# Performance work log

Measured on AMD Instinct MI355X. Metric: run time of the kernel, lower is better.

The kernel has to match this reference:

```python
import jax, jax.numpy as jnp
import numpy as np
from functools import partial

L, B, D_IN, D_MODEL, D_OUT, D_STATE = 2048, 8, 128, 256, 32, 16
D_INNER, DT_RANK, K_CONV = 2 * D_MODEL, D_MODEL // 16, 4
LOG2PI = float(np.log(2.0 * np.pi))


def setup_inputs() -> dict:
    key = jax.random.key(0)
    ks = jax.random.split(key, 16)
    sc = 0.02
    inp = {
        "s": jax.random.normal(ks[0], (L, B, D_IN), jnp.float32),
        "a": jax.random.normal(ks[1], (L, B, D_OUT), jnp.float32),
        # embedding linear
        "W_emb": jax.random.normal(ks[2], (D_IN, D_MODEL), jnp.float32) * sc,
        "b_emb": jnp.zeros((D_MODEL,), jnp.float32),
        # mamba block params
        "norm_w": jnp.ones((D_MODEL,), jnp.float32),
        "W_in": jax.random.normal(ks[3], (D_MODEL, 2 * D_INNER), jnp.float32) * sc,
        "conv_w": jax.random.normal(ks[4], (D_INNER, 1, K_CONV), jnp.float32) * sc,
        "conv_b": jnp.zeros((D_INNER,), jnp.float32),
        "W_x": jax.random.normal(ks[5], (D_INNER, DT_RANK + 2 * D_STATE), jnp.float32) * sc,
        "W_dt": jax.random.normal(ks[6], (DT_RANK, D_INNER), jnp.float32) * sc,
        "b_dt": jnp.full((D_INNER,), -2.0, jnp.float32),  # softplus(-2) ~ small init dt
        "A_log": jnp.broadcast_to(jnp.log(jnp.arange(1, D_STATE + 1, dtype=jnp.float32)), (D_INNER, D_STATE)).copy(),
        "D": jnp.ones((D_INNER,), jnp.float32),
        "W_out": jax.random.normal(ks[7], (D_INNER, D_MODEL), jnp.float32) * sc,
        # action head + log_std
        "W_head": jax.random.normal(ks[8], (D_MODEL, D_OUT), jnp.float32) * sc,
        "b_head": jnp.zeros((D_OUT,), jnp.float32),
        "log_std": jnp.zeros((D_OUT,), jnp.float32),
    }
    return inp


def _rmsnorm(x, w, eps=1e-5):
    return x * jax.lax.rsqrt(jnp.mean(x * x, axis=-1, keepdims=True) + eps) * w


def _silu(x):
    return x * jax.nn.sigmoid(x)


def _mamba_block(x, norm_w, W_in, conv_w, conv_b, W_x, W_dt, b_dt, A_log, D, W_out):
    # x: (B, L, d_model)
    resid = x
    xn = _rmsnorm(x, norm_w)
    xz = xn @ W_in                                  # (B, L, 2*d_inner)
    xp, z = jnp.split(xz, 2, axis=-1)
    # causal depthwise conv over time
    xc = jax.lax.conv_general_dilated(
        xp.transpose(0, 2, 1), conv_w, window_strides=(1,),
        padding=[(K_CONV - 1, 0)], feature_group_count=D_INNER,
        dimension_numbers=("NCH", "OIH", "NCH"))
    xp = _silu((xc + conv_b[None, :, None]).transpose(0, 2, 1))  # (B, L, d_inner)
    # input-dependent SSM params
    x_dbl = xp @ W_x                                # (B, L, dt_rank + 2*d_state)
    dt, Bm, Cm = jnp.split(x_dbl, [DT_RANK, DT_RANK + D_STATE], axis=-1)
    dt = jax.nn.softplus(dt @ W_dt + b_dt)          # (B, L, d_inner)
    A = -jnp.exp(A_log)                             # (d_inner, d_state)

    def step(h, t):
        dt_t, B_t, C_t, x_t = t                     # (B,d_i) (B,d_s) (B,d_s) (B,d_i)
        dA = jnp.exp(dt_t[..., None] * A)           # (B, d_inner, d_state)
        dBx = (dt_t * x_t)[..., None] * B_t[:, None, :]
        h = dA * h + dBx
        y = jnp.einsum("bds,bs->bd", h, C_t)
        return h, y

    h0 = jnp.zeros((x.shape[0], D_INNER, D_STATE), x.dtype)
    tm = lambda u: jnp.moveaxis(u, 1, 0)            # time-major
    _, ys = jax.lax.scan(step, h0, (tm(dt), tm(Bm), tm(Cm), tm(xp)))
    y = jnp.moveaxis(ys, 0, 1) + xp * D             # (B, L, d_inner)
    y = y * _silu(z)
    return y @ W_out + resid


def reference(s, a, W_emb, b_emb, norm_w, W_in, conv_w, conv_b, W_x, W_dt, b_dt,
              A_log, D, W_out, W_head, b_head, log_std):
    x = s @ W_emb + b_emb                           # (L, B, d_model)
    x = x.transpose(1, 0, 2)                        # (B, L, d_model)
    x = _mamba_block(x, norm_w, W_in, conv_w, conv_b, W_x, W_dt, b_dt, A_log, D, W_out)
    x = x.transpose(1, 0, 2)                        # (L, B, d_model)
    mu = x @ W_head + b_head                        # (L, B, d_out)
    # Normal(mu, exp(log_std)).log_prob(a).sum(-1)
    z = (a - mu) * jnp.exp(-log_std)
    logp = -0.5 * z * z - log_std - 0.5 * LOG2PI
    return logp.sum(axis=-1)                        # (L, B)
```

## Files before the change

### kernel.cpp

```cpp
#include <hip/hip_runtime.h>

typedef unsigned short u16;
typedef short bf16x8 __attribute__((ext_vector_type(8)));
typedef float floatx4 __attribute__((ext_vector_type(4)));

#define LSEQ 2048
#define BB 8
#define NTOK (LSEQ*BB)
#define DMODEL 256
#define DINNER 512
#define NSEG 128
#define SEGLEN 16

__device__ __forceinline__ float siluf(float x){ return x / (1.f + __expf(-x)); }
__device__ __forceinline__ float b2f(u16 x){ return __uint_as_float(((unsigned)x) << 16); }
__device__ __forceinline__ u16 f2b(float f){
  unsigned u = __float_as_uint(f);
  unsigned r = (u + 0x7fffu + ((u >> 16) & 1u)) >> 16;
  return (u16)r;
}

__global__ __launch_bounds__(256) void prep_k(
    const float* __restrict__ Wemb, const float* __restrict__ Win,
    const float* __restrict__ Wout, const float* __restrict__ Wx,
    const float* __restrict__ Wdt, const float* __restrict__ Wh,
    u16* __restrict__ WTe, u16* __restrict__ WTi, u16* __restrict__ WTo,
    u16* __restrict__ WxT, u16* __restrict__ WdtTp, u16* __restrict__ WhT)
{
  int g = blockIdx.x, tid = threadIdx.x;
  if (g < 128) {
    int idx = g*256 + tid; int n = idx >> 7, k = idx & 127;
    WTe[idx] = f2b(Wemb[(size_t)k*256 + n]);
  } else if (g < 1152) {
    int idx = (g-128)*256 + tid; int n = idx >> 8, k = idx & 255;
    WTi[idx] = f2b(Win[(size_t)k*1024 + n]);
  } else if (g < 1664) {
    int idx = (g-1152)*256 + tid; int n = idx >> 9, k = idx & 511;
    WTo[idx] = f2b(Wout[(size_t)k*256 + n]);
  } else if (g < 1760) {
    int idx = (g-1664)*256 + tid; int n = idx >> 9, k = idx & 511;
    WxT[idx] = f2b(Wx[(size_t)k*48 + n]);
  } else if (g < 1824) {
    int idx = (g-1760)*256 + tid; int c = idx >> 5, r = idx & 31;
    WdtTp[idx] = (r < 16) ? f2b(Wdt[(size_t)r*512 + c]) : (u16)0;
  } else {
    int idx = (g-1824)*256 + tid; int j = idx >> 8, k = idx & 255;
    WhT[idx] = f2b(Wh[(size_t)k*32 + j]);
  }
}

__global__ __launch_bounds__(256) void embnorm_k(
    const float* __restrict__ s, const u16* __restrict__ WTe,
    const float* __restrict__ bemb, const float* __restrict__ nw,
    u16* __restrict__ Xb, u16* __restrict__ XNb)
{
  __shared__ u16 SH[64*264];
  __shared__ float ssq[64*4];
  __shared__ float rr[64];
  u16* As = SH;
  u16* Bs = SH + 64*40;
  const int tid = threadIdx.x;
  const int wave = tid >> 6, lane = tid & 63;
  const int quad = lane >> 4, l16 = lane & 15;
  const int m0 = blockIdx.x*64;
  const int wn = wave*64;
  const int srow = tid >> 2, sch = (tid & 3)*8;
  floatx4 acc[4][4];
  #pragma unroll
  for (int r = 0; r < 4; ++r)
    #pragma unroll
    for (int c = 0; c < 4; ++c) acc[r][c] = (floatx4){0.f,0.f,0.f,0.f};

  for (int k0 = 0; k0 < 128; k0 += 32) {
    {
      float4 v0 = *(const float4*)&s[(size_t)(m0+srow)*128 + k0 + sch];
      float4 v1 = *(const float4*)&s[(size_t)(m0+srow)*128 + k0 + sch + 4];
      __align__(16) u16 o[8];
      o[0]=f2b(v0.x); o[1]=f2b(v0.y); o[2]=f2b(v0.z); o[3]=f2b(v0.w);
      o[4]=f2b(v1.x); o[5]=f2b(v1.y); o[6]=f2b(v1.z); o[7]=f2b(v1.w);
      *(uint4*)&As[srow*40 + sch] = *(const uint4*)o;
    }
    #pragma unroll
    for (int p = 0; p < 4; ++p) {
      int row = srow + p*64;
      *(uint4*)&Bs[row*40 + sch] = *(const uint4*)&WTe[(size_t)row*128 + k0 + sch];
    }
    __syncthreads();
    bf16x8 af[4], bf[4];
    #pragma unroll
    for (int r = 0; r < 4; ++r) af[r] = *(const bf16x8*)&As[(r*16 + l16)*40 + quad*8];
    #pragma unroll
    for (int c = 0; c < 4; ++c) bf[c] = *(const bf16x8*)&Bs[(wn + c*16 + l16)*40 + quad*8];
    #pragma unroll
    for (int r = 0; r < 4; ++r)
      #pragma unroll
      for (int c = 0; c < 4; ++c)
        acc[r][c] = __builtin_amdgcn_mfma_f32_16x16x32_bf16(af[r], bf[c], acc[r][c], 0, 0, 0);
    __syncthreads();
  }
  u16* Xs = SH;
  #pragma unroll
  for (int c = 0; c < 4; ++c) {
    int n = wn + c*16 + l16;
    float bv = bemb[n];
    #pragma unroll
    for (int r = 0; r < 4; ++r)
      #pragma unroll
      for (int reg = 0; reg < 4; ++reg) {
        int ml = r*16 + quad*4 + reg;
        Xs[ml*264 + n] = f2b(acc[r][c][reg] + bv);
      }
  }
  __syncthreads();
  #pragma unroll
  for (int p = 0; p < 8; ++p) {
    int row = p*8 + (tid >> 5);
    int col = (tid & 31)*8;
    *(uint4*)&Xb[(size_t)(m0+row)*256 + col] = *(const uint4*)&Xs[row*264 + col];
  }
  const int tk = tid >> 2, q = tid & 3;
  float ss = 0.f;
  #pragma unroll
  for (int j = 0; j < 8; ++j) {
    uint4 v = *(const uint4*)&Xs[tk*264 + q*64 + j*8];
    const u16* u = (const u16*)&v;
    #pragma unroll
    for (int i = 0; i < 8; ++i) { float x = b2f(u[i]); ss += x*x; }
  }
  ssq[tk*4 + q] = ss;
  __syncthreads();
  if (q == 0)
    rr[tk] = rsqrtf((ssq[tk*4]+ssq[tk*4+1]+ssq[tk*4+2]+ssq[tk*4+3])*(1.f/DMODEL) + 1e-5f);
  __syncthreads();
  float r = rr[tk];
  #pragma unroll
  for (int j = 0; j < 8; ++j) {
    int idx = q*64 + j*8;
    uint4 v = *(const uint4*)&Xs[tk*264 + idx];
    const u16* u = (const u16*)&v;
    float4 w0 = *(const float4*)&nw[idx];
    float4 w1 = *(const float4*)&nw[idx+4];
    __align__(16) u16 o[8];
    o[0]=f2b(b2f(u[0])*r*w0.x); o[1]=f2b(b2f(u[1])*r*w0.y);
    o[2]=f2b(b2f(u[2])*r*w0.z); o[3]=f2b(b2f(u[3])*r*w0.w);
    o[4]=f2b(b2f(u[4])*r*w1.x); o[5]=f2b(b2f(u[5])*r*w1.y);
    o[6]=f2b(b2f(u[6])*r*w1.z); o[7]=f2b(b2f(u[7])*r*w1.w);
    *(uint4*)&XNb[(size_t)(m0+tk)*256 + idx] = *(const uint4*)o;
  }
}

template<int K>
__global__ __launch_bounds__(256) void gemm_mfma(
    const u16* __restrict__ Ab, const u16* __restrict__ WT,
    u16* __restrict__ Cv, int N)
{
  __shared__ u16 SH[128*136];
  u16* As = SH;
  u16* Bs = SH + 128*40;
  const int tid = threadIdx.x;
  const int wave = tid >> 6, lane = tid & 63;
  const int quad = lane >> 4, l16 = lane & 15;
  const int bm0 = blockIdx.x*128, bn0 = blockIdx.y*128;
  const int wm = (wave & 1)*64, wn = (wave >> 1)*64;
  const int srow = tid >> 2, sch = (tid & 3)*8;
  floatx4 acc[4][4];
  #pragma unroll
  for (int r = 0; r < 4; ++r)
    #pragma unroll
    for (int c = 0; c < 4; ++c) acc[r][c] = (floatx4){0.f,0.f,0.f,0.f};

  for (int k0 = 0; k0 < K; k0 += 32) {
    #pragma unroll
    for (int p = 0; p < 2; ++p) {
      int row = srow + p*64;
      *(uint4*)&As[row*40 + sch] = *(const uint4*)&Ab[(size_t)(bm0+row)*K + k0 + sch];
      *(uint4*)&Bs[row*40 + sch] = *(const uint4*)&WT[(size_t)(bn0+row)*K + k0 + sch];
    }
    __syncthreads();
    bf16x8 af[4], bf[4];
    #pragma unroll
    for (int r = 0; r < 4; ++r) af[r] = *(const bf16x8*)&As[(wm + r*16 + l16)*40 + quad*8];
    #pragma unroll
    for (int c = 0; c < 4; ++c) bf[c] = *(const bf16x8*)&Bs[(wn + c*16 + l16)*40 + quad*8];
    #pragma unroll
    for (int r = 0; r < 4; ++r)
      #pragma unroll
      for (int c = 0; c < 4; ++c)
        acc[r][c] = __builtin_amdgcn_mfma_f32_16x16x32_bf16(af[r], bf[c], acc[r][c], 0, 0, 0);
    __syncthreads();
  }
  u16* Cs = SH;
  #pragma unroll
  for (int c = 0; c < 4; ++c) {
    int nl = wn + c*16 + l16;
    #pragma unroll
    for (int r = 0; r < 4; ++r)
      #pragma unroll
      for (int reg = 0; reg < 4; ++reg) {
        int ml = wm + r*16 + quad*4 + reg;
        Cs[ml*136 + nl] = f2b(acc[r][c][reg]);
      }
  }
  __syncthreads();
  #pragma unroll
  for (int p = 0; p < 8; ++p) {
    int row = p*16 + (tid >> 4);
    int col = (tid & 15)*8;
    uint4 v = *(const uint4*)&Cs[row*136 + col];
    *(uint4*)&Cv[(size_t)(bm0+row)*N + bn0 + col] = v;
  }
}

__global__ __launch_bounds__(256) void xdblBC_k(const u16* __restrict__ XZb,
    const float* __restrict__ cw, const float* __restrict__ cb,
    const u16* __restrict__ WxT,
    float* __restrict__ BM, float* __restrict__ CM, u16* __restrict__ DTRb)
{
  __shared__ u16 As[64*40];
  __shared__ u16 Ws[48*40];
  __shared__ float CWs[512*4];
  __shared__ float CBs[512];
  const int tid = threadIdx.x;
  const int wave = tid >> 6, lane = tid & 63;
  const int quad = lane >> 4, l16 = lane & 15;
  const int m0 = blockIdx.x*64;
  const int srow = tid >> 2, sch = (tid & 3)*8;
  const int n = m0 + srow;
  for (int e = tid; e < 2048; e += 256) CWs[e] = cw[e];
  for (int e = tid; e < 512;  e += 256) CBs[e] = cb[e];
  floatx4 acc[3];
  #pragma unroll
  for (int j = 0; j < 3; ++j) acc[j] = (floatx4){0.f,0.f,0.f,0.f};
  __syncthreads();
  const bf16x8 z8 = {0,0,0,0,0,0,0,0};
  for (int k0 = 0; k0 < DINNER; k0 += 32) {
    bf16x8 t3 = *(const bf16x8*)&XZb[(size_t)n*1024 + k0 + sch];
    bf16x8 t2 = z8, t1 = z8, t0v = z8;
    if (n >= 8)  t2  = *(const bf16x8*)&XZb[(size_t)(n-8)*1024  + k0 + sch];
    if (n >= 16) t1  = *(const bf16x8*)&XZb[(size_t)(n-16)*1024 + k0 + sch];
    if (n >= 24) t0v = *(const bf16x8*)&XZb[(size_t)(n-24)*1024 + k0 + sch];
    __align__(16) u16 outa[8];
    #pragma unroll
    for (int j = 0; j < 8; ++j) {
      int c = k0 + sch + j;
      float4 wv = *(const float4*)&CWs[c*4];
      float xc = CBs[c] + wv.x*b2f((u16)t0v[j]) + wv.y*b2f((u16)t1[j])
               + wv.z*b2f((u16)t2[j]) + wv.w*b2f((u16)t3[j]);
      outa[j] = f2b(siluf(xc));
    }
    *(uint4*)&As[srow*40 + sch] = *(const uint4*)outa;
    if (tid < 192) {
      int wr = tid >> 2;
      *(uint4*)&Ws[wr*40 + sch] = *(const uint4*)&WxT[(size_t)wr*512 + k0 + sch];
    }
    __syncthreads();
    bf16x8 af = *(const bf16x8*)&As[(wave*16 + l16)*40 + quad*8];
    #pragma unroll
    for (int j = 0; j < 3; ++j) {
      bf16x8 bf = *(const bf16x8*)&Ws[(j*16 + l16)*40 + quad*8];
      acc[j] = __builtin_amdgcn_mfma_f32_16x16x32_bf16(af, bf, acc[j], 0, 0, 0);
    }
    __syncthreads();
  }
  const int tok0 = m0 + wave*16;
  #pragma unroll
  for (int reg = 0; reg < 4; ++reg) {
    size_t t = (size_t)(tok0 + quad*4 + reg);
    BM[t*16 + l16] = acc[1][reg];
    CM[t*16 + l16] = acc[2][reg];
    DTRb[t*32 + l16]      = f2b(acc[0][reg]);
    DTRb[t*32 + 16 + l16] = 0;
  }
}

__global__ __launch_bounds__(256) void dtg_k(const u16* __restrict__ DTRb,
    const u16* __restrict__ WdtTp, const float* __restrict__ bdt,
    u16* __restrict__ DTb)
{
  __shared__ u16 Cs[128*136];
  const int tid = threadIdx.x;
  const int wave = tid >> 6, lane = tid & 63;
  const int quad = lane >> 4, l16 = lane & 15;
  const int bm0 = blockIdx.x*128, bn0 = blockIdx.y*128;
  const int bm = bm0 + (wave & 1)*64;
  const int bn = bn0 + (wave >> 1)*64;
  bf16x8 af[4], bf[4];
  #pragma unroll
  for (int r = 0; r < 4; ++r)
    af[r] = *(const bf16x8*)(DTRb + (size_t)(bm + r*16 + l16)*32 + quad*8);
  #pragma unroll
  for (int c = 0; c < 4; ++c)
    bf[c] = *(const bf16x8*)(WdtTp + (size_t)(bn + c*16 + l16)*32 + quad*8);
  #pragma unroll
  for (int c = 0; c < 4; ++c) {
    int nl = (wave >> 1)*64 + c*16 + l16;
    float bd = bdt[bn0 + nl];
    #pragma unroll
    for (int r = 0; r < 4; ++r) {
      floatx4 d = __builtin_amdgcn_mfma_f32_16x16x32_bf16(af[r], bf[c],
                    (floatx4){0.f,0.f,0.f,0.f}, 0, 0, 0);
      #pragma unroll
      for (int reg = 0; reg < 4; ++reg) {
        int ml = (wave & 1)*64 + r*16 + quad*4 + reg;
        float sum = d[reg] + bd;
        Cs[ml*136 + nl] = f2b((sum > 20.f) ? sum : __logf(1.f + __expf(sum)));
      }
    }
  }
  __syncthreads();
  #pragma unroll
  for (int p = 0; p < 8; ++p) {
    int row = p*16 + (tid >> 4);
    int col = (tid & 15)*8;
    uint4 v = *(const uint4*)&Cs[row*136 + col];
    *(uint4*)&DTb[(size_t)(bm0+row)*DINNER + bn0 + col] = v;
  }
}

__global__ __launch_bounds__(256) void scanA_k(const u16* __restrict__ DTb,
    const u16* __restrict__ XZb, const float* __restrict__ BM,
    const float* __restrict__ cw, const float* __restrict__ cb,
    const float* __restrict__ Alog, u16* __restrict__ HENDb, float* __restrict__ DTS)
{
  __shared__ __align__(16) float Bs[SEGLEN*16];
  const int tid = threadIdx.x;
  const int seg = blockIdx.x, b = blockIdx.y, half = blockIdx.z;
  const int c = half*256 + tid;
  const int t0 = seg*SEGLEN;
  {
    int t = tid >> 4, s = tid & 15;
    Bs[tid] = BM[((size_t)(t0+t)*BB + b)*16 + s];
  }
  float As[16];
  #pragma unroll
  for (int s = 0; s < 16; ++s) As[s] = -__expf(Alog[c*16+s]);
  bool uni = true;
  #pragma unroll
  for (int s = 1; s < 16; ++s)
    uni = uni && (fabsf(As[s] - As[0]*(float)(s+1)) <= 1e-4f*(float)(s+1));
  const float4 cwv = *(const float4*)&cw[c*4];
  const float cbv = cb[c];
  float h[16];
  #pragma unroll
  for (int s = 0; s < 16; ++s) h[s] = 0.f;
  float dts = 0.f;
  __syncthreads();
  const size_t base = (size_t)t0*BB + b;
  const u16* dtp = DTb + base*DINNER + c;
  const u16* xzp = XZb + base*1024 + c;
  float w0 = (t0 >= 3) ? b2f(xzp[-(size_t)3*BB*1024]) : 0.f;
  float w1 = (t0 >= 2) ? b2f(xzp[-(size_t)2*BB*1024]) : 0.f;
  float w2 = (t0 >= 1) ? b2f(xzp[-(size_t)1*BB*1024]) : 0.f;
  float dt = b2f(dtp[0]);
  float xz = b2f(xzp[0]);
  for (int t = 0; t < SEGLEN; ++t) {
    float dtn = 0.f, xzn = 0.f;
    if (t+1 < SEGLEN) {
      dtn = b2f(dtp[(size_t)(t+1)*BB*DINNER]);
      xzn = b2f(xzp[(size_t)(t+1)*BB*1024]);
    }
    float xp = siluf(cbv + cwv.x*w0 + cwv.y*w1 + cwv.z*w2 + cwv.w*xz);
    w0 = w1; w1 = w2; w2 = xz;
    dts += dt;
    float dtx = dt * xp;
    const float4 b0 = *(const float4*)&Bs[t*16+0];
    const float4 b1 = *(const float4*)&Bs[t*16+4];
    const float4 b2 = *(const float4*)&Bs[t*16+8];
    const float4 b3 = *(const float4*)&Bs[t*16+12];
    const float bv[16] = {b0.x,b0.y,b0.z,b0.w, b1.x,b1.y,b1.z,b1.w,
                          b2.x,b2.y,b2.z,b2.w, b3.x,b3.y,b3.z,b3.w};
    float dA[16];
    if (uni) {
      float p = __expf(dt*As[0]);
      dA[0] = p;
      #pragma unroll
      for (int s = 1; s < 16; ++s) dA[s] = dA[s-1]*p;
    } else {
      #pragma unroll
      for (int s = 0; s < 16; ++s) dA[s] = __expf(dt*As[s]);
    }
    #pragma unroll
    for (int s = 0; s < 16; ++s)
      h[s] = fmaf(dA[s], h[s], dtx*bv[s]);
    dt = dtn; xz = xzn;
  }
  u16* hp = &HENDb[(((size_t)seg*BB + b)*DINNER + c)*16];
  #pragma unroll
  for (int q = 0; q < 2; ++q) {
    ushort4 v0, v1;
    v0.x = f2b(h[q*8+0]); v0.y = f2b(h[q*8+1]); v0.z = f2b(h[q*8+2]); v0.w = f2b(h[q*8+3]);
    v1.x = f2b(h[q*8+4]); v1.y = f2b(h[q*8+5]); v1.z = f2b(h[q*8+6]); v1.w = f2b(h[q*8+7]);
    *(ushort4*)&hp[q*8]     = v0;
    *(ushort4*)&hp[q*8 + 4] = v1;
  }
  DTS[((size_t)seg*BB + b)*DINNER + c] = dts;
}

__global__ __launch_bounds__(256) void stitch_k(u16* __restrict__ HENDb,
    const float* __restrict__ DTS, const float* __restrict__ Alog)
{
  int g = blockIdx.x*256 + threadIdx.x;
  int b = g >> 13;
  int rem = g & 8191;
  int cidx = rem >> 4;
  float A = -__expf(Alog[rem]);
  float h0 = 0.f;
  for (int k = 0; k < NSEG; ++k) {
    size_t idx = (((size_t)k*BB + b) << 13) + rem;
    float hend = b2f(HENDb[idx]);
    HENDb[idx] = f2b(h0);
    float dts = DTS[((size_t)k*BB + b)*DINNER + cidx];
    h0 = fmaf(__expf(dts*A), h0, hend);
  }
}

__global__ __launch_bounds__(256) void scanC_k(const u16* __restrict__ DTb,
    const u16* __restrict__ XZb, const float* __restrict__ BM, const float* __restrict__ CM,
    const float* __restrict__ cw, const float* __restrict__ cb,
    const float* __restrict__ Alog, const float* __restrict__ Dp,
    const u16* __restrict__ H0b, u16* __restrict__ YGb)
{
  __shared__ __align__(16) float Bs[SEGLEN*16];
  __shared__ __align__(16) float Cs[SEGLEN*16];
  const int tid = threadIdx.x;
  const int seg = blockIdx.x, b = blockIdx.y, half = blockIdx.z;
  const int c = half*256 + tid;
  const int t0 = seg*SEGLEN;
  {
    int t = tid >> 4, s = tid & 15;
    size_t nb = ((size_t)(t0+t)*BB + b)*16 + s;
    Bs[tid] = BM[nb];
    Cs[tid] = CM[nb];
  }
  float As[16];
  #pragma unroll
  for (int s = 0; s < 16; ++s) As[s] = -__expf(Alog[c*16+s]);
  bool uni = true;
  #pragma unroll
  for (int s = 1; s < 16; ++s)
    uni = uni && (fabsf(As[s] - As[0]*(float)(s+1)) <= 1e-4f*(float)(s+1));
  const float4 cwv = *(const float4*)&cw[c*4];
  const float cbv = cb[c];
  float h[16];
  const u16* hp = &H0b[(((size_t)seg*BB + b)*DINNER + c)*16];
  #pragma unroll
  for (int q = 0; q < 4; ++q) {
    ushort4 hv = *(const ushort4*)&hp[q*4];
    h[q*4+0]=b2f(hv.x); h[q*4+1]=b2f(hv.y); h[q*4+2]=b2f(hv.z); h[q*4+3]=b2f(hv.w);
  }
  const float Dv = Dp[c];
  __syncthreads();
  const size_t base = (size_t)t0*BB + b;
  const u16* dtp = DTb + base*DINNER + c;
  const u16* xzp = XZb + base*1024 + c;
  const u16* zp  = XZb + base*1024 + DINNER + c;
  u16*       ygp = YGb + base*DINNER + c;
  float w0 = (t0 >= 3) ? b2f(xzp[-(size_t)3*BB*1024]) : 0.f;
  float w1 = (t0 >= 2) ? b2f(xzp[-(size_t)2*BB*1024]) : 0.f;
  float w2 = (t0 >= 1) ? b2f(xzp[-(size_t)1*BB*1024]) : 0.f;
  float dt = b2f(dtp[0]);
  float xz = b2f(xzp[0]);
  float zg = b2f(zp[0]);
  for (int t = 0; t < SEGLEN; ++t) {
    float dtn = 0.f, xzn = 0.f, zgn = 0.f;
    if (t+1 < SEGLEN) {
      dtn = b2f(dtp[(size_t)(t+1)*BB*DINNER]);
      xzn = b2f(xzp[(size_t)(t+1)*BB*1024]);
      zgn = b2f(zp[(size_t)(t+1)*BB*1024]);
    }
    float xp = siluf(cbv + cwv.x*w0 + cwv.y*w1 + cwv.z*w2 + cwv.w*xz);
    w0 = w1; w1 = w2; w2 = xz;
    float dtx = dt * xp;
    const float4 b0 = *(const float4*)&Bs[t*16+0];
    const float4 b1 = *(const float4*)&Bs[t*16+4];
    const float4 b2 = *(const float4*)&Bs[t*16+8];
    const float4 b3 = *(const float4*)&Bs[t*16+12];
    const float4 c0 = *(const float4*)&Cs[t*16+0];
    const float4 c1 = *(const float4*)&Cs[t*16+4];
    const float4 c2 = *(const float4*)&Cs[t*16+8];
    const float4 c3 = *(const float4*)&Cs[t*16+12];
    const float bvv[16] = {b0.x,b0.y,b0.z,b0.w, b1.x,b1.y,b1.z,b1.w,
                           b2.x,b2.y,b2.z,b2.w, b3.x,b3.y,b3.z,b3.w};
    const float cvv[16] = {c0.x,c0.y,c0.z,c0.w, c1.x,c1.y,c1.z,c1.w,
                           c2.x,c2.y,c2.z,c2.w, c3.x,c3.y,c3.z,c3.w};
    float dA[16];
    if (uni) {
      float p = __expf(dt*As[0]);
      dA[0] = p;
      #pragma unroll
      for (int s = 1; s < 16; ++s) dA[s] = dA[s-1]*p;
    } else {
      #pragma unroll
      for (int s = 0; s < 16; ++s) dA[s] = __expf(dt*As[s]);
    }
    float y0 = 0.f, y1 = 0.f, y2 = 0.f, y3 = 0.f;
    #pragma unroll
    for (int q = 0; q < 4; ++q) {
      h[q*4+0] = fmaf(dA[q*4+0], h[q*4+0], dtx*bvv[q*4+0]);
      h[q*4+1] = fmaf(dA[q*4+1], h[q*4+1], dtx*bvv[q*4+1]);
      h[q*4+2] = fmaf(dA[q*4+2], h[q*4+2], dtx*bvv[q*4+2]);
      h[q*4+3] = fmaf(dA[q*4+3], h[q*4+3], dtx*bvv[q*4+3]);
      y0 = fmaf(h[q*4+0], cvv[q*4+0], y0);
      y1 = fmaf(h[q*4+1], cvv[q*4+1], y1);
      y2 = fmaf(h[q*4+2], cvv[q*4+2], y2);
      y3 = fmaf(h[q*4+3], cvv[q*4+3], y3);
    }
    float y = (y0+y1) + (y2+y3);
    ygp[(size_t)t*BB*DINNER] = f2b((y + xp*Dv) * siluf(zg));
    dt = dtn; xz = xzn; zg = zgn;
  }
}

__global__ __launch_bounds__(256) void outhead_k(const u16* __restrict__ YGb,
    const u16* __restrict__ WTo, const u16* __restrict__ Xb,
    const u16* __restrict__ WhT, const float* __restrict__ bh,
    const float* __restrict__ lstd, const float* __restrict__ a,
    float* __restrict__ out)
{
  __shared__ u16 Xs[64*264];
  u16* As = Xs;
  u16* Bs = Xs + 64*40;
  const int tid = threadIdx.x;
  const int wave = tid >> 6, lane = tid & 63;
  const int quad = lane >> 4, l16 = lane & 15;
  const int m0 = blockIdx.x*64;
  const int n0 = wave*64;
  const int srow = tid >> 2, sch = (tid & 3)*8;
  floatx4 acc[4][4];
  #pragma unroll
  for (int r = 0; r < 4; ++r)
    #pragma unroll
    for (int c = 0; c < 4; ++c) acc[r][c] = (floatx4){0.f,0.f,0.f,0.f};

  for (int k0 = 0; k0 < DINNER; k0 += 32) {
    if (srow < 64)
      *(uint4*)&As[srow*40 + sch] = *(const uint4*)&YGb[(size_t)(m0+srow)*DINNER + k0 + sch];
    #pragma unroll
    for (int p = 0; p < 4; ++p) {
      int row = srow + p*64;
      *(uint4*)&Bs[row*40 + sch] = *(const uint4*)&WTo[(size_t)row*DINNER + k0 + sch];
    }
    __syncthreads();
    bf16x8 af[4], bf[4];
    #pragma unroll
    for (int r = 0; r < 4; ++r) af[r] = *(const bf16x8*)&As[(r*16 + l16)*40 + quad*8];
    #pragma unroll
    for (int c = 0; c < 4; ++c) bf[c] = *(const bf16x8*)&Bs[(n0 + c*16 + l16)*40 + quad*8];
    #pragma unroll
    for (int r = 0; r < 4; ++r)
      #pragma unroll
      for (int c = 0; c < 4; ++c)
        acc[r][c] = __builtin_amdgcn_mfma_f32_16x16x32_bf16(af[r], bf[c], acc[r][c], 0, 0, 0);
    __syncthreads();
  }
  #pragma unroll
  for (int p = 0; p < 8; ++p) {
    int row = p*8 + (tid >> 5);
    int col = (tid & 31)*8;
    *(uint4*)&Xs[row*264 + col] = *(const uint4*)&Xb[(size_t)(m0+row)*256 + col];
  }
  __syncthreads();
  #pragma unroll
  for (int c = 0; c < 4; ++c) {
    int n = n0 + c*16 + l16;
    #pragma unroll
    for (int r = 0; r < 4; ++r) {
      #pragma unroll
      for (int reg = 0; reg < 4; ++reg) {
        int ml = r*16 + quad*4 + reg;
        Xs[ml*264 + n] = f2b(acc[r][c][reg] + b2f(Xs[ml*264 + n]));
      }
    }
  }
  __syncthreads();
  floatx4 mu[2];
  mu[0] = (floatx4){0.f,0.f,0.f,0.f};
  mu[1] = (floatx4){0.f,0.f,0.f,0.f};
  #pragma unroll
  for (int k0 = 0; k0 < DMODEL; k0 += 32) {
    bf16x8 axf = *(const bf16x8*)&Xs[(wave*16 + l16)*264 + k0 + quad*8];
    #pragma unroll
    for (int nt = 0; nt < 2; ++nt) {
      bf16x8 bwf = *(const bf16x8*)(WhT + (size_t)(nt*16 + l16)*DMODEL + k0 + quad*8);
      mu[nt] = __builtin_amdgcn_mfma_f32_16x16x32_bf16(axf, bwf, mu[nt], 0, 0, 0);
    }
  }
  float ls0 = lstd[l16],      els0 = __expf(-ls0), bh0 = bh[l16];
  float ls1 = lstd[16 + l16], els1 = __expf(-ls1), bh1 = bh[16 + l16];
  #pragma unroll
  for (int reg = 0; reg < 4; ++reg) {
    int tok = m0 + wave*16 + quad*4 + reg;
    float m0v = mu[0][reg] + bh0;
    float m1v = mu[1][reg] + bh1;
    float z0 = (a[(size_t)tok*32 + l16]      - m0v) * els0;
    float z1 = (a[(size_t)tok*32 + 16 + l16] - m1v) * els1;
    float t = (-0.5f*z0*z0 - ls0) + (-0.5f*z1*z1 - ls1) - 2.f*0.91893853320467274f;
    t += __shfl_xor(t, 1);
    t += __shfl_xor(t, 2);
    t += __shfl_xor(t, 4);
    t += __shfl_xor(t, 8);
    if (l16 == 0) out[tok] = t;
  }
}

extern "C" void kernel_launch(void* const* d_in, const int* in_sizes, int n_in,
                              void* d_out, int out_size, void* d_ws, size_t ws_size,
                              hipStream_t stream)
{
  const float* s    = (const float*)d_in[0];
  const float* a    = (const float*)d_in[1];
  const float* Wemb = (const float*)d_in[2];
  const float* bemb = (const float*)d_in[3];
  const float* nw   = (const float*)d_in[4];
  const float* Win  = (const float*)d_in[5];
  const float* cw   = (const float*)d_in[6];
  const float* cb   = (const float*)d_in[7];
  const float* Wx   = (const float*)d_in[8];
  const float* Wdt  = (const float*)d_in[9];
  const float* bdt  = (const float*)d_in[10];
  const float* Alog = (const float*)d_in[11];
  const float* Dp   = (const float*)d_in[12];
  const float* Wout = (const float*)d_in[13];
  const float* Wh   = (const float*)d_in[14];
  const float* bh   = (const float*)d_in[15];
  const float* lstd = (const float*)d_in[16];

  u16*   Xb   = (u16*)d_ws;
  u16*   XZb  = Xb  + (size_t)NTOK*DMODEL;
  u16*   XNb  = XZb + (size_t)NTOK*1024;
  u16*   DTb  = XNb + (size_t)NTOK*DMODEL;
  u16*   YGb  = DTb + (size_t)NTOK*DINNER;
  u16*   WTe  = YGb + (size_t)NTOK*DINNER;
  u16*   WTi  = WTe + 256*128;
  u16*   WTo  = WTi + 1024*256;
  u16*   WxT  = WTo + 256*512;
  u16*   WdtTp= WxT + 48*512;
  u16*   WhT  = WdtTp + 512*32;
  u16*   DTRb = WhT + 32*256;
  u16*   HENDb= DTRb + (size_t)NTOK*32;
  float* BM   = (float*)(HENDb + (size_t)NSEG*BB*DINNER*16);
  float* CM   = BM + (size_t)NTOK*16;
  float* DTS  = CM + (size_t)NTOK*16;
  float* out  = (float*)d_out;

  prep_k       <<<1856,        256, 0, stream>>>(Wemb, Win, Wout, Wx, Wdt, Wh,
                                                 WTe, WTi, WTo, WxT, WdtTp, WhT);
  embnorm_k    <<<256,         256, 0, stream>>>(s, WTe, bemb, nw, Xb, XNb);
  gemm_mfma<256><<<dim3(128,8), 256, 0, stream>>>(XNb, WTi, XZb, 1024);
  xdblBC_k     <<<256,         256, 0, stream>>>(XZb, cw, cb, WxT, BM, CM, DTRb);
  dtg_k        <<<dim3(128,4), 256, 0, stream>>>(DTRb, WdtTp, bdt, DTb);
  scanA_k      <<<dim3(NSEG,BB,2), 256, 0, stream>>>(DTb, XZb, BM, cw, cb, Alog, HENDb, DTS);
  stitch_k     <<<256,         256, 0, stream>>>(HENDb, DTS, Alog);
  scanC_k      <<<dim3(NSEG,BB,2), 256, 0, stream>>>(DTb, XZb, BM, CM, cw, cb, Alog, Dp, HENDb, YGb);
  outhead_k    <<<256,         256, 0, stream>>>(YGb, WTo, Xb, WhT, bh, lstd, a, out);
}
```

Before: 247.8 us.

## Fuse dt projection and softplus into scan kernels; widen GEMM K-tile to 64

Removes the separate dtg_k kernel and its bf16 DT buffer, which was a 16K x 512 intermediate. Each scan thread now recomputes dt from the fp32 low-rank DTR (16 values per token, held in shared memory) and its own column of W_dt, followed by softplus. This trades a large global write and two reads of DT for 16 FMAs plus exp/log per step in both scan passes. Separately, the main GEMM and the out/head GEMM now load 64-wide K tiles with a 72-element padded LDS stride, halving the number of barrier iterations.

```diff
diff --git a/kernel.cpp b/kernel.cpp
--- a/kernel.cpp
+++ b/kernel.cpp
@@ -23,9 +23,9 @@
 __global__ __launch_bounds__(256) void prep_k(
     const float* __restrict__ Wemb, const float* __restrict__ Win,
     const float* __restrict__ Wout, const float* __restrict__ Wx,
-    const float* __restrict__ Wdt, const float* __restrict__ Wh,
+    const float* __restrict__ Wh,
     u16* __restrict__ WTe, u16* __restrict__ WTi, u16* __restrict__ WTo,
-    u16* __restrict__ WxT, u16* __restrict__ WdtTp, u16* __restrict__ WhT)
+    u16* __restrict__ WxT, u16* __restrict__ WhT)
 {
   int g = blockIdx.x, tid = threadIdx.x;
   if (g < 128) {
@@ -40,11 +40,8 @@
   } else if (g < 1760) {
     int idx = (g-1664)*256 + tid; int n = idx >> 9, k = idx & 511;
     WxT[idx] = f2b(Wx[(size_t)k*48 + n]);
-  } else if (g < 1824) {
-    int idx = (g-1760)*256 + tid; int c = idx >> 5, r = idx & 31;
-    WdtTp[idx] = (r < 16) ? f2b(Wdt[(size_t)r*512 + c]) : (u16)0;
   } else {
-    int idx = (g-1824)*256 + tid; int j = idx >> 8, k = idx & 255;
+    int idx = (g-1760)*256 + tid; int j = idx >> 8, k = idx & 255;
     WhT[idx] = f2b(Wh[(size_t)k*32 + j]);
   }
 }
@@ -154,39 +151,44 @@
     const u16* __restrict__ Ab, const u16* __restrict__ WT,
     u16* __restrict__ Cv, int N)
 {
-  __shared__ u16 SH[128*136];
+  __shared__ u16 SH[2*128*72];
   u16* As = SH;
-  u16* Bs = SH + 128*40;
+  u16* Bs = SH + 128*72;
   const int tid = threadIdx.x;
   const int wave = tid >> 6, lane = tid & 63;
   const int quad = lane >> 4, l16 = lane & 15;
   const int bm0 = blockIdx.x*128, bn0 = blockIdx.y*128;
   const int wm = (wave & 1)*64, wn = (wave >> 1)*64;
-  const int srow = tid >> 2, sch = (tid & 3)*8;
+  const int srow = tid >> 3, sch = (tid & 7)*8;
   floatx4 acc[4][4];
   #pragma unroll
   for (int r = 0; r < 4; ++r)
     #pragma unroll
     for (int c = 0; c < 4; ++c) acc[r][c] = (floatx4){0.f,0.f,0.f,0.f};
 
-  for (int k0 = 0; k0 < K; k0 += 32) {
-    #pragma unroll
-    for (int p = 0; p < 2; ++p) {
-      int row = srow + p*64;
-      *(uint4*)&As[row*40 + sch] = *(const uint4*)&Ab[(size_t)(bm0+row)*K + k0 + sch];
-      *(uint4*)&Bs[row*40 + sch] = *(const uint4*)&WT[(size_t)(bn0+row)*K + k0 + sch];
-    }
-    __syncthreads();
-    bf16x8 af[4], bf[4];
-    #pragma unroll
-    for (int r = 0; r < 4; ++r) af[r] = *(const bf16x8*)&As[(wm + r*16 + l16)*40 + quad*8];
-    #pragma unroll
-    for (int c = 0; c < 4; ++c) bf[c] = *(const bf16x8*)&Bs[(wn + c*16 + l16)*40 + quad*8];
-    #pragma unroll
-    for (int r = 0; r < 4; ++r)
+  for (int k0 = 0; k0 < K; k0 += 64) {
+    #pragma unroll
+    for (int p = 0; p < 4; ++p) {
+      int row = srow + p*32;
+      *(uint4*)&As[row*72 + sch] = *(const uint4*)&Ab[(size_t)(bm0+row)*K + k0 + sch];
+      *(uint4*)&Bs[row*72 + sch] = *(const uint4*)&WT[(size_t)(bn0+row)*K + k0 + sch];
+    }
+    __syncthreads();
+    #pragma unroll
+    for (int ks = 0; ks < 2; ++ks) {
+      bf16x8 af[4], bf[4];
+      #pragma unroll
+      for (int r = 0; r < 4; ++r)
+        af[r] = *(const bf16x8*)&As[(wm + r*16 + l16)*72 + ks*32 + quad*8];
       #pragma unroll
       for (int c = 0; c < 4; ++c)
-        acc[r][c] = __builtin_amdgcn_mfma_f32_16x16x32_bf16(af[r], bf[c], acc[r][c], 0, 0, 0);
+        bf[c] = *(const bf16x8*)&Bs[(wn + c*16 + l16)*72 + ks*32 + quad*8];
+      #pragma unroll
+      for (int r = 0; r < 4; ++r)
+        #pragma unroll
+        for (int c = 0; c < 4; ++c)
+          acc[r][c] = __builtin_amdgcn_mfma_f32_16x16x32_bf16(af[r], bf[c], acc[r][c], 0, 0, 0);
+    }
     __syncthreads();
   }
   u16* Cs = SH;
@@ -214,7 +216,7 @@
 __global__ __launch_bounds__(256) void xdblBC_k(const u16* __restrict__ XZb,
     const float* __restrict__ cw, const float* __restrict__ cb,
     const u16* __restrict__ WxT,
-    float* __restrict__ BM, float* __restrict__ CM, u16* __restrict__ DTRb)
+    float* __restrict__ BM, float* __restrict__ CM, float* __restrict__ DTR)
 {
   __shared__ u16 As[64*40];
   __shared__ u16 Ws[48*40];
@@ -266,70 +268,29 @@
   #pragma unroll
   for (int reg = 0; reg < 4; ++reg) {
     size_t t = (size_t)(tok0 + quad*4 + reg);
-    BM[t*16 + l16] = acc[1][reg];
-    CM[t*16 + l16] = acc[2][reg];
-    DTRb[t*32 + l16]      = f2b(acc[0][reg]);
-    DTRb[t*32 + 16 + l16] = 0;
-  }
-}
-
-__global__ __launch_bounds__(256) void dtg_k(const u16* __restrict__ DTRb,
-    const u16* __restrict__ WdtTp, const float* __restrict__ bdt,
-    u16* __restrict__ DTb)
-{
-  __shared__ u16 Cs[128*136];
-  const int tid = threadIdx.x;
-  const int wave = tid >> 6, lane = tid & 63;
-  const int quad = lane >> 4, l16 = lane & 15;
-  const int bm0 = blockIdx.x*128, bn0 = blockIdx.y*128;
-  const int bm = bm0 + (wave & 1)*64;
-  const int bn = bn0 + (wave >> 1)*64;
-  bf16x8 af[4], bf[4];
-  #pragma unroll
-  for (int r = 0; r < 4; ++r)
-    af[r] = *(const bf16x8*)(DTRb + (size_t)(bm + r*16 + l16)*32 + quad*8);
-  #pragma unroll
-  for (int c = 0; c < 4; ++c)
-    bf[c] = *(const bf16x8*)(WdtTp + (size_t)(bn + c*16 + l16)*32 + quad*8);
-  #pragma unroll
-  for (int c = 0; c < 4; ++c) {
-    int nl = (wave >> 1)*64 + c*16 + l16;
-    float bd = bdt[bn0 + nl];
-    #pragma unroll
-    for (int r = 0; r < 4; ++r) {
-      floatx4 d = __builtin_amdgcn_mfma_f32_16x16x32_bf16(af[r], bf[c],
-                    (floatx4){0.f,0.f,0.f,0.f}, 0, 0, 0);
-      #pragma unroll
-      for (int reg = 0; reg < 4; ++reg) {
-        int ml = (wave & 1)*64 + r*16 + quad*4 + reg;
-        float sum = d[reg] + bd;
-        Cs[ml*136 + nl] = f2b((sum > 20.f) ? sum : __logf(1.f + __expf(sum)));
-      }
-    }
-  }
-  __syncthreads();
-  #pragma unroll
-  for (int p = 0; p < 8; ++p) {
-    int row = p*16 + (tid >> 4);
-    int col = (tid & 15)*8;
-    uint4 v = *(const uint4*)&Cs[row*136 + col];
-    *(uint4*)&DTb[(size_t)(bm0+row)*DINNER + bn0 + col] = v;
-  }
-}
-
-__global__ __launch_bounds__(256) void scanA_k(const u16* __restrict__ DTb,
+    BM[t*16 + l16]  = acc[1][reg];
+    CM[t*16 + l16]  = acc[2][reg];
+    DTR[t*16 + l16] = acc[0][reg];
+  }
+}
+
+__global__ __launch_bounds__(256) void scanA_k(const float* __restrict__ DTR,
     const u16* __restrict__ XZb, const float* __restrict__ BM,
     const float* __restrict__ cw, const float* __restrict__ cb,
+    const float* __restrict__ Wdt, const float* __restrict__ bdt,
     const float* __restrict__ Alog, u16* __restrict__ HENDb, float* __restrict__ DTS)
 {
   __shared__ __align__(16) float Bs[SEGLEN*16];
+  __shared__ __align__(16) float DRs[SEGLEN*16];
   const int tid = threadIdx.x;
   const int seg = blockIdx.x, b = blockIdx.y, half = blockIdx.z;
   const int c = half*256 + tid;
   const int t0 = seg*SEGLEN;
   {
     int t = tid >> 4, s = tid & 15;
-    Bs[tid] = BM[((size_t)(t0+t)*BB + b)*16 + s];
+    size_t nb = ((size_t)(t0+t)*BB + b)*16 + s;
+    Bs[tid]  = BM[nb];
+    DRs[tid] = DTR[nb];
   }
   float As[16];
   #pragma unroll
@@ -338,6 +299,10 @@
   #pragma unroll
   for (int s = 1; s < 16; ++s)
     uni = uni && (fabsf(As[s] - As[0]*(float)(s+1)) <= 1e-4f*(float)(s+1));
+  float wdt[16];
+  #pragma unroll
+  for (int r = 0; r < 16; ++r) wdt[r] = Wdt[r*DINNER + c];
+  const float bd = bdt[c];
   const float4 cwv = *(const float4*)&cw[c*4];
   const float cbv = cb[c];
   float h[16];
@@ -346,19 +311,18 @@
   float dts = 0.f;
   __syncthreads();
   const size_t base = (size_t)t0*BB + b;
-  const u16* dtp = DTb + base*DINNER + c;
   const u16* xzp = XZb + base*1024 + c;
   float w0 = (t0 >= 3) ? b2f(xzp[-(size_t)3*BB*1024]) : 0.f;
   float w1 = (t0 >= 2) ? b2f(xzp[-(size_t)2*BB*1024]) : 0.f;
   float w2 = (t0 >= 1) ? b2f(xzp[-(size_t)1*BB*1024]) : 0.f;
-  float dt = b2f(dtp[0]);
   float xz = b2f(xzp[0]);
   for (int t = 0; t < SEGLEN; ++t) {
-    float dtn = 0.f, xzn = 0.f;
-    if (t+1 < SEGLEN) {
-      dtn = b2f(dtp[(size_t)(t+1)*BB*DINNER]);
-      xzn = b2f(xzp[(size_t)(t+1)*BB*1024]);
-    }
+    float xzn = 0.f;
+    if (t+1 < SEGLEN) xzn = b2f(xzp[(size_t)(t+1)*BB*1024]);
+    float dsum = bd;
+    #pragma unroll
+    for (int r = 0; r < 16; ++r) dsum = fmaf(DRs[t*16+r], wdt[r], dsum);
+    float dt = (dsum > 20.f) ? dsum : __logf(1.f + __expf(dsum));
     float xp = siluf(cbv + cwv.x*w0 + cwv.y*w1 + cwv.z*w2 + cwv.w*xz);
     w0 = w1; w1 = w2; w2 = xz;
     dts += dt;
@@ -382,7 +346,7 @@
     #pragma unroll
     for (int s = 0; s < 16; ++s)
       h[s] = fmaf(dA[s], h[s], dtx*bv[s]);
-    dt = dtn; xz = xzn;
+    xz = xzn;
   }
   u16* hp = &HENDb[(((size_t)seg*BB + b)*DINNER + c)*16];
   #pragma unroll
@@ -414,14 +378,16 @@
   }
 }
 
-__global__ __launch_bounds__(256) void scanC_k(const u16* __restrict__ DTb,
+__global__ __launch_bounds__(256) void scanC_k(const float* __restrict__ DTR,
     const u16* __restrict__ XZb, const float* __restrict__ BM, const float* __restrict__ CM,
     const float* __restrict__ cw, const float* __restrict__ cb,
+    const float* __restrict__ Wdt, const float* __restrict__ bdt,
     const float* __restrict__ Alog, const float* __restrict__ Dp,
     const u16* __restrict__ H0b, u16* __restrict__ YGb)
 {
   __shared__ __align__(16) float Bs[SEGLEN*16];
   __shared__ __align__(16) float Cs[SEGLEN*16];
+  __shared__ __align__(16) float DRs[SEGLEN*16];
   const int tid = threadIdx.x;
   const int seg = blockIdx.x, b = blockIdx.y, half = blockIdx.z;
   const int c = half*256 + tid;
@@ -429,8 +395,9 @@
   {
     int t = tid >> 4, s = tid & 15;
     size_t nb = ((size_t)(t0+t)*BB + b)*16 + s;
-    Bs[tid] = BM[nb];
-    Cs[tid] = CM[nb];
+    Bs[tid]  = BM[nb];
+    Cs[tid]  = CM[nb];
+    DRs[tid] = DTR[nb];
   }
   float As[16];
   #pragma unroll
@@ -439,6 +406,10 @@
   #pragma unroll
   for (int s = 1; s < 16; ++s)
     uni = uni && (fabsf(As[s] - As[0]*(float)(s+1)) <= 1e-4f*(float)(s+1));
+  float wdt[16];
+  #pragma unroll
+  for (int r = 0; r < 16; ++r) wdt[r] = Wdt[r*DINNER + c];
+  const float bd = bdt[c];
   const float4 cwv = *(const float4*)&cw[c*4];
   const float cbv = cb[c];
   float h[16];
@@ -451,23 +422,24 @@
   const float Dv = Dp[c];
   __syncthreads();
   const size_t base = (size_t)t0*BB + b;
-  const u16* dtp = DTb + base*DINNER + c;
   const u16* xzp = XZb + base*1024 + c;
   const u16* zp  = XZb + base*1024 + DINNER + c;
   u16*       ygp = YGb + base*DINNER + c;
   float w0 = (t0 >= 3) ? b2f(xzp[-(size_t)3*BB*1024]) : 0.f;
   float w1 = (t0 >= 2) ? b2f(xzp[-(size_t)2*BB*1024]) : 0.f;
   float w2 = (t0 >= 1) ? b2f(xzp[-(size_t)1*BB*1024]) : 0.f;
-  float dt = b2f(dtp[0]);
   float xz = b2f(xzp[0]);
   float zg = b2f(zp[0]);
   for (int t = 0; t < SEGLEN; ++t) {
-    float dtn = 0.f, xzn = 0.f, zgn = 0.f;
+    float xzn = 0.f, zgn = 0.f;
     if (t+1 < SEGLEN) {
-      dtn = b2f(dtp[(size_t)(t+1)*BB*DINNER]);
       xzn = b2f(xzp[(size_t)(t+1)*BB*1024]);
       zgn = b2f(zp[(size_t)(t+1)*BB*1024]);
     }
+    float dsum = bd;
+    #pragma unroll
+    for (int r = 0; r < 16; ++r) dsum = fmaf(DRs[t*16+r], wdt[r], dsum);
+    float dt = (dsum > 20.f) ? dsum : __logf(1.f + __expf(dsum));
     float xp = siluf(cbv + cwv.x*w0 + cwv.y*w1 + cwv.z*w2 + cwv.w*xz);
     w0 = w1; w1 = w2; w2 = xz;
     float dtx = dt * xp;
@@ -507,7 +479,7 @@
     }
     float y = (y0+y1) + (y2+y3);
     ygp[(size_t)t*BB*DINNER] = f2b((y + xp*Dv) * siluf(zg));
-    dt = dtn; xz = xzn; zg = zgn;
+    xz = xzn; zg = zgn;
   }
 }
 
@@ -517,42 +489,51 @@
     const float* __restrict__ lstd, const float* __restrict__ a,
     float* __restrict__ out)
 {
-  __shared__ u16 Xs[64*264];
-  u16* As = Xs;
-  u16* Bs = Xs + 64*40;
+  __shared__ u16 SH[(64+256)*72];
+  u16* As = SH;
+  u16* Bs = SH + 64*72;
   const int tid = threadIdx.x;
   const int wave = tid >> 6, lane = tid & 63;
   const int quad = lane >> 4, l16 = lane & 15;
   const int m0 = blockIdx.x*64;
   const int n0 = wave*64;
-  const int srow = tid >> 2, sch = (tid & 3)*8;
+  const int srow = tid >> 3, sch = (tid & 7)*8;
   floatx4 acc[4][4];
   #pragma unroll
   for (int r = 0; r < 4; ++r)
     #pragma unroll
     for (int c = 0; c < 4; ++c) acc[r][c] = (floatx4){0.f,0.f,0.f,0.f};
 
-  for (int k0 = 0; k0 < DINNER; k0 += 32) {
-    if (srow < 64)
-      *(uint4*)&As[srow*40 + sch] = *(const uint4*)&YGb[(size_t)(m0+srow)*DINNER + k0 + sch];
-    #pragma unroll
-    for (int p = 0; p < 4; ++p) {
-      int row = srow + p*64;
-      *(uint4*)&Bs[row*40 + sch] = *(const uint4*)&WTo[(size_t)row*DINNER + k0 + sch];
-    }
-    __syncthreads();
-    bf16x8 af[4], bf[4];
-    #pragma unroll
-    for (int r = 0; r < 4; ++r) af[r] = *(const bf16x8*)&As[(r*16 + l16)*40 + quad*8];
-    #pragma unroll
-    for (int c = 0; c < 4; ++c) bf[c] = *(const bf16x8*)&Bs[(n0 + c*16 + l16)*40 + quad*8];
-    #pragma unroll
-    for (int r = 0; r < 4; ++r)
+  for (int k0 = 0; k0 < DINNER; k0 += 64) {
+    #pragma unroll
+    for (int p = 0; p < 2; ++p) {
+      int row = srow + p*32;
+      *(uint4*)&As[row*72 + sch] = *(const uint4*)&YGb[(size_t)(m0+row)*DINNER + k0 + sch];
+    }
+    #pragma unroll
+    for (int p = 0; p < 8; ++p) {
+      int row = srow + p*32;
+      *(uint4*)&Bs[row*72 + sch] = *(const uint4*)&WTo[(size_t)row*DINNER + k0 + sch];
+    }
+    __syncthreads();
+    #pragma unroll
+    for (int ks = 0; ks < 2; ++ks) {
+      bf16x8 af[4], bf[4];
+      #pragma unroll
+      for (int r = 0; r < 4; ++r)
+        af[r] = *(const bf16x8*)&As[(r*16 + l16)*72 + ks*32 + quad*8];
       #pragma unroll
       for (int c = 0; c < 4; ++c)
-        acc[r][c] = __builtin_amdgcn_mfma_f32_16x16x32_bf16(af[r], bf[c], acc[r][c], 0, 0, 0);
-    __syncthreads();
-  }
+        bf[c] = *(const bf16x8*)&Bs[(n0 + c*16 + l16)*72 + ks*32 + quad*8];
+      #pragma unroll
+      for (int r = 0; r < 4; ++r)
+        #pragma unroll
+        for (int c = 0; c < 4; ++c)
+          acc[r][c] = __builtin_amdgcn_mfma_f32_16x16x32_bf16(af[r], bf[c], acc[r][c], 0, 0, 0);
+    }
+    __syncthreads();
+  }
+  u16* Xs = SH;
   #pragma unroll
   for (int p = 0; p < 8; ++p) {
     int row = p*8 + (tid >> 5);
@@ -628,29 +609,28 @@
   u16*   Xb   = (u16*)d_ws;
   u16*   XZb  = Xb  + (size_t)NTOK*DMODEL;
   u16*   XNb  = XZb + (size_t)NTOK*1024;
-  u16*   DTb  = XNb + (size_t)NTOK*DMODEL;
-  u16*   YGb  = DTb + (size_t)NTOK*DINNER;
+  u16*   YGb  = XNb + (size_t)NTOK*DMODEL;
   u16*   WTe  = YGb + (size_t)NTOK*DINNER;
   u16*   WTi  = WTe + 256*128;
   u16*   WTo  = WTi + 1024*256;
   u16*   WxT  = WTo + 256*512;
-  u16*   WdtTp= WxT + 48*512;
-  u16*   WhT  = WdtTp + 512*32;
-  u16*   DTRb = WhT + 32*256;
-  u16*   HENDb= DTRb + (size_t)NTOK*32;
+  u16*   WhT  = WxT + 48*512;
+  u16*   HENDb= WhT + 32*256;
   float* BM   = (float*)(HENDb + (size_t)NSEG*BB*DINNER*16);
   float* CM   = BM + (size_t)NTOK*16;
-  float* DTS  = CM + (size_t)NTOK*16;
+  float* DTR  = CM + (size_t)NTOK*16;
+  float* DTS  = DTR + (size_t)NTOK*16;
   float* out  = (float*)d_out;
 
-  prep_k       <<<1856,        256, 0, stream>>>(Wemb, Win, Wout, Wx, Wdt, Wh,
-                                                 WTe, WTi, WTo, WxT, WdtTp, WhT);
-  embnorm_k    <<<256,         256, 0, stream>>>(s, WTe, bemb, nw, Xb, XNb);
+  prep_k        <<<1792,        256, 0, stream>>>(Wemb, Win, Wout, Wx, Wh,
+                                                  WTe, WTi, WTo, WxT, WhT);
+  embnorm_k     <<<256,         256, 0, stream>>>(s, WTe, bemb, nw, Xb, XNb);
   gemm_mfma<256><<<dim3(128,8), 256, 0, stream>>>(XNb, WTi, XZb, 1024);
-  xdblBC_k     <<<256,         256, 0, stream>>>(XZb, cw, cb, WxT, BM, CM, DTRb);
-  dtg_k        <<<dim3(128,4), 256, 0, stream>>>(DTRb, WdtTp, bdt, DTb);
-  scanA_k      <<<dim3(NSEG,BB,2), 256, 0, stream>>>(DTb, XZb, BM, cw, cb, Alog, HENDb, DTS);
-  stitch_k     <<<256,         256, 0, stream>>>(HENDb, DTS, Alog);
-  scanC_k      <<<dim3(NSEG,BB,2), 256, 0, stream>>>(DTb, XZb, BM, CM, cw, cb, Alog, Dp, HENDb, YGb);
-  outhead_k    <<<256,         256, 0, stream>>>(YGb, WTo, Xb, WhT, bh, lstd, a, out);
-}
+  xdblBC_k      <<<256,         256, 0, stream>>>(XZb, cw, cb, WxT, BM, CM, DTR);
+  scanA_k       <<<dim3(NSEG,BB,2), 256, 0, stream>>>(DTR, XZb, BM, cw, cb, Wdt, bdt,
+                                                      Alog, HENDb, DTS);
+  stitch_k      <<<256,         256, 0, stream>>>(HENDb, DTS, Alog);
+  scanC_k       <<<dim3(NSEG,BB,2), 256, 0, stream>>>(DTR, XZb, BM, CM, cw, cb, Wdt, bdt,
+                                                      Alog, Dp, HENDb, YGb);
+  outhead_k     <<<256,         256, 0, stream>>>(YGb, WTo, Xb, WhT, bh, lstd, a, out);
+}
```

New measurement: 251.4 us. Within noise of the previous version (+1.5%).
